# Optimization experiments

Hardware: AMD Instinct MI355X
Metric: run time of the kernel (lower is better)

The kernel has to match this reference:

```python
import jax, jax.numpy as jnp
import numpy as np

NCHARS = 50000
NWORDS = 500000
NIC = 64      # ninput_char
NIW = 64      # ninput_word
NH = 128      # nhidden
NA = 5        # naction (nmapping_fn)
B = 65536     # batch size


def setup_inputs() -> dict:
    key = jax.random.key(0)
    ks = jax.random.split(key, 12)
    s = 0.05
    return {
        "x": jax.random.randint(ks[0], (B, 2), 0, NCHARS),
        "y": jax.random.randint(ks[1], (B,), 0, NWORDS),
        "cemb_table": jax.random.normal(ks[2], (NCHARS, NIC), jnp.float32) * s,
        "wemb_table": jax.random.normal(ks[3], (NWORDS, NIW), jnp.float32) * s,
        # Policy MLP: Linear(2*NIC -> NH), ReLU, Linear(NH -> NA), Softmax
        "Wp1": jax.random.normal(ks[4], (2 * NIC, NH), jnp.float32) * s,
        "bp1": jnp.zeros((NH,), jnp.float32),
        "Wp2": jax.random.normal(ks[5], (NH, NA), jnp.float32) * s,
        "bp2": jnp.zeros((NA,), jnp.float32),
        # NA expert MLPs, stacked: Linear(2*NIC -> NH), ReLU, Linear(NH -> NIW)
        "We1": jax.random.normal(ks[6], (NA, 2 * NIC, NH), jnp.float32) * s,
        "be1": jnp.zeros((NA, NH), jnp.float32),
        "We2": jax.random.normal(ks[7], (NA, NH, NIW), jnp.float32) * s,
        "be2": jnp.zeros((NA, NIW), jnp.float32),
    }


def reference(x, y, cemb_table, wemb_table, Wp1, bp1, Wp2, bp2, We1, be1, We2, be2):
    bsize = x.shape[0]
    # char_embs(x).view(bsize, -1): [B, 2*NIC]
    cembs = cemb_table[x].reshape(bsize, -1)

    # Policy (dropout off in eval): probs = softmax(relu(cembs@Wp1+bp1)@Wp2+bp2)
    # Categorical sampling over probs == categorical over the pre-softmax logits.
    logits = jnp.maximum(cembs @ Wp1 + bp1, 0.0) @ Wp2 + bp2
    action = jax.random.categorical(jax.random.key(42), logits)   # [B]
    action_mask = jax.nn.one_hot(action, NA, dtype=cembs.dtype)   # [B, NA]

    # Dense evaluation of all NA experts (matches the Python loop + stack)
    h = jnp.maximum(jnp.einsum('bd,adh->bah', cembs, We1) + be1, 0.0)  # [B, NA, NH]
    mapped = jnp.einsum('bah,aho->bao', h, We2) + be2                  # [B, NA, NIW]

    # sum(unsqueeze(mask,-1) * mapped, dim=1)
    out = jnp.einsum('ba,bao->bo', action_mask, mapped)               # [B, NIW]

    wemb = wemb_table[y]                                              # [B, NIW]
    return (out, wemb)
```

## Files before the change

### kernel.cpp

```cpp
#include <hip/hip_runtime.h>
#include <stdint.h>

#define B_N   65536
#define NIC   64
#define NIW   64
#define NH    128
#define NA    5
#define D2    128

#define PARTITIONABLE 1

#define P2_NCHUNK 51
#define P2_R      1286

typedef __attribute__((ext_vector_type(8))) short short8;
typedef __attribute__((ext_vector_type(4))) float f32x4;

__device__ __forceinline__ ushort f2bf(float f) {
  uint32_t u = __float_as_uint(f);
  uint32_t r = (u + 0x7FFFu + ((u >> 16) & 1u)) >> 16;
  return (ushort)r;
}

__device__ __forceinline__ void split2(float f, ushort& h, ushort& l) {
  h = f2bf(f);
  l = f2bf(f - __uint_as_float(((uint32_t)h) << 16));
}

__device__ __forceinline__ void threefry2x32_k042(uint32_t x0, uint32_t x1,
                                                  uint32_t& o0, uint32_t& o1) {
  const uint32_t ks0 = 0u;
  const uint32_t ks1 = 42u;
  const uint32_t ks2 = 0x1BD11BDAu ^ 0u ^ 42u;
  x0 += ks0; x1 += ks1;
#define TF_RND(r) { x0 += x1; x1 = (x1 << (r)) | (x1 >> (32 - (r))); x1 ^= x0; }
  TF_RND(13) TF_RND(15) TF_RND(26) TF_RND(6)
  x0 += ks1; x1 += ks2 + 1u;
  TF_RND(17) TF_RND(29) TF_RND(16) TF_RND(24)
  x0 += ks2; x1 += ks0 + 2u;
  TF_RND(13) TF_RND(15) TF_RND(26) TF_RND(6)
  x0 += ks0; x1 += ks1 + 3u;
  TF_RND(17) TF_RND(29) TF_RND(16) TF_RND(24)
  x0 += ks1; x1 += ks2 + 4u;
  TF_RND(13) TF_RND(15) TF_RND(26) TF_RND(6)
  x0 += ks2; x1 += ks0 + 5u;
#undef TF_RND
  o0 = x0; o1 = x1;
}

__device__ __forceinline__ float gumbel_at(uint32_t idx) {
  uint32_t bits;
#if PARTITIONABLE
  uint32_t a, b;
  threefry2x32_k042(0u, idx, a, b);
  bits = a ^ b;
#else
  const uint32_t HALF = (uint32_t)(B_N * NA) / 2u;
  uint32_t a, b;
  if (idx < HALF) { threefry2x32_k042(idx, idx + HALF, a, b); bits = a; }
  else            { threefry2x32_k042(idx - HALF, idx, a, b); bits = b; }
#endif
  const float f = __uint_as_float((bits >> 9) | 0x3f800000u) - 1.0f;
  const double u = (f == 0.0f) ? (double)0x1p-126 : (double)f;
  const float nl = (float)(-log(u));
  const float g  = (float)(-log((double)nl));
  return g;
}

__global__ __launch_bounds__(512, 4) void policy_kernel(
    const int* __restrict__ x, const int* __restrict__ y,
    const float* __restrict__ cemb, const float* __restrict__ wemb,
    const float* __restrict__ Wp1, const float* __restrict__ bp1,
    const float* __restrict__ Wp2, const float* __restrict__ bp2,
    float* __restrict__ out_wemb, int* __restrict__ action) {
  __shared__ __align__(16) ushort sW1h[16384];
  __shared__ __align__(16) ushort sW1l[16384];
  __shared__ __align__(16) float sW2t[NA][NH];
  __shared__ __align__(16) float sb1[NH];
  __shared__ __align__(16) float sbp2[8];

  const int tid = threadIdx.x;
  const int base = blockIdx.x * 128;

  {
    const int n = tid & 127, q = tid >> 7;
    const int fb = (n >> 4) * 4 + q;
    const int cc = n & 15;
#pragma unroll
    for (int grp = 0; grp < 4; grp++) {
      short8 ph, pl;
#pragma unroll
      for (int j = 0; j < 8; j++) {
        const int k = 32 * q + 8 * grp + j;
        ushort hh, ll;
        split2(Wp1[k * NH + n], hh, ll);
        ph[j] = (short)hh;
        pl[j] = (short)ll;
      }
      *(short8*)&sW1h[fb * 512 + (cc + 16 * grp) * 8] = ph;
      *(short8*)&sW1l[fb * 512 + (cc + 16 * grp) * 8] = pl;
    }
    if (tid < NH) sb1[tid] = bp1[tid];
    if (tid < NA * 32) {
      const int a = tid >> 5, k0 = (tid & 31) * 4;
#pragma unroll
      for (int j = 0; j < 4; j++) sW2t[a][k0 + j] = Wp2[(k0 + j) * NA + a];
    }
    if (tid < NA) sbp2[tid] = bp2[tid];
  }

  const int wave = tid >> 6, lane = tid & 63;
  const int c16 = lane & 15, h2 = lane >> 4;

  const int grow = base + wave * 16 + c16;
  const int xi0 = x[grow * 2], xi1 = x[grow * 2 + 1];
  short8 Ah[4], Al[4];
#pragma unroll
  for (int kt = 0; kt < 4; kt++) {
    const int xi = (kt < 2) ? xi0 : xi1;
    const float* src = cemb + (size_t)xi * NIC + (kt & 1) * 32 + h2 * 8;
    const float4 aa = *(const float4*)src;
    const float4 bb = *(const float4*)(src + 4);
    ushort hh, ll;
    short8 ph, pl;
    split2(aa.x, hh, ll); ph[0] = (short)hh; pl[0] = (short)ll;
    split2(aa.y, hh, ll); ph[1] = (short)hh; pl[1] = (short)ll;
    split2(aa.z, hh, ll); ph[2] = (short)hh; pl[2] = (short)ll;
    split2(aa.w, hh, ll); ph[3] = (short)hh; pl[3] = (short)ll;
    split2(bb.x, hh, ll); ph[4] = (short)hh; pl[4] = (short)ll;
    split2(bb.y, hh, ll); ph[5] = (short)hh; pl[5] = (short)ll;
    split2(bb.z, hh, ll); ph[6] = (short)hh; pl[6] = (short)ll;
    split2(bb.w, hh, ll); ph[7] = (short)hh; pl[7] = (short)ll;
    Ah[kt] = ph;
    Al[kt] = pl;
  }
  __syncthreads();

  float part[4][5];
#pragma unroll
  for (int r = 0; r < 4; r++)
#pragma unroll
    for (int a = 0; a < NA; a++) part[r][a] = 0.0f;

#pragma unroll
  for (int half = 0; half < 2; half++) {
    f32x4 acc[4];
#pragma unroll
    for (int c2 = 0; c2 < 4; c2++) {
      const float bv = sb1[(half * 4 + c2) * 16 + c16];
      acc[c2] = (f32x4){bv, bv, bv, bv};
    }
#pragma unroll
    for (int kt = 0; kt < 4; kt++) {
#pragma unroll
      for (int c2 = 0; c2 < 4; c2++) {
        const int fb = (half * 4 + c2) * 4 + kt;
        const short8 Bh = *(const short8*)&sW1h[fb * 512 + lane * 8];
        const short8 Bl = *(const short8*)&sW1l[fb * 512 + lane * 8];
        acc[c2] = __builtin_amdgcn_mfma_f32_16x16x32_bf16(Ah[kt], Bh, acc[c2], 0, 0, 0);
        acc[c2] = __builtin_amdgcn_mfma_f32_16x16x32_bf16(Al[kt], Bh, acc[c2], 0, 0, 0);
        acc[c2] = __builtin_amdgcn_mfma_f32_16x16x32_bf16(Ah[kt], Bl, acc[c2], 0, 0, 0);
      }
    }
#pragma unroll
    for (int c2 = 0; c2 < 4; c2++) {
      const int ct = half * 4 + c2;
      float w[NA];
#pragma unroll
      for (int a = 0; a < NA; a++) w[a] = sW2t[a][ct * 16 + c16];
#pragma unroll
      for (int r = 0; r < 4; r++) {
        const float hv = fmaxf(acc[c2][r], 0.0f);
#pragma unroll
        for (int a = 0; a < NA; a++) part[r][a] = fmaf(hv, w[a], part[r][a]);
      }
    }
  }

#pragma unroll
  for (int st = 1; st <= 8; st <<= 1) {
#pragma unroll
    for (int r = 0; r < 4; r++)
#pragma unroll
      for (int a = 0; a < NA; a++)
        part[r][a] += __shfl_xor(part[r][a], st);
  }

  float score0, score1;
  {
    const int r0_ = c16 / 5, a0_ = c16 - 5 * (c16 / 5);
    float lg = 0.0f;
#pragma unroll
    for (int r = 0; r < 4; r++)
#pragma unroll
      for (int a = 0; a < NA; a++)
        if (r0_ == r && a0_ == a) lg = part[r][a];
    const float logit = lg + sbp2[a0_];
    const int growr = base + wave * 16 + h2 * 4 + r0_;
    score0 = gumbel_at((uint32_t)(growr * NA + a0_)) + logit;
  }
  {
    const int a1_ = (c16 & 3) + 1;
    float lg = 0.0f;
#pragma unroll
    for (int a = 1; a < NA; a++)
      if (a1_ == a) lg = part[3][a];
    const float logit = lg + sbp2[a1_];
    const int growr = base + wave * 16 + h2 * 4 + 3;
    score1 = gumbel_at((uint32_t)(growr * NA + a1_)) + logit;
  }

  int best = 0;
  float bs = 0.0f;
#pragma unroll
  for (int a = 0; a < NA; a++) {
    const int idx = c16 * 5 + a;
    const int src = h2 * 16 + ((idx < 16) ? idx : (idx - 16));
    const float v0 = __shfl(score0, src);
    const float v1 = __shfl(score1, src);
    const float s = (idx < 16) ? v0 : v1;
    if (a == 0) bs = s;
    else if (s > bs) { bs = s; best = a; }
  }
  if (c16 < 4) action[base + wave * 16 + h2 * 4 + c16] = best;

#pragma unroll 1
  for (int i = tid; i < 128 * 16; i += 512) {
    const int row = i >> 4, seg = i & 15;
    ((float4*)out_wemb)[(size_t)(base + row) * 16 + seg] =
        ((const float4*)wemb)[(size_t)y[base + row] * 16 + seg];
  }
}

__global__ __launch_bounds__(512, 1) void expert_staged(
    const int* __restrict__ x, const float* __restrict__ cemb,
    const float* __restrict__ We1, const float* __restrict__ be1,
    const float* __restrict__ We2, const float* __restrict__ be2,
    const int* __restrict__ action, float* __restrict__ out) {
  __shared__ __align__(16) ushort sW1[16384];
  __shared__ __align__(16) ushort sW2[8192];
  __shared__ __align__(16) ushort sHt[8][2048];
  __shared__ __align__(16) float sbe1[NH];
  __shared__ __align__(16) float sbe2[NIW];
  __shared__ int sList[P2_R];
  __shared__ int sCount;

  const int tid = threadIdx.x;
  const int a = blockIdx.x % NA;
  const int chunk = blockIdx.x / NA;
  const int rowBeg = chunk * P2_R;
  const int rowEnd = (rowBeg + P2_R < B_N) ? rowBeg + P2_R : B_N;

  const int wave = tid >> 6, lane = tid & 63;

  if (tid == 0) sCount = 0;
  __syncthreads();

  for (int r0 = rowBeg; r0 < rowEnd; r0 += 512) {
    const int r = r0 + tid;
    const bool m = (r < rowEnd) && (action[r] == a);
    const unsigned long long mask = __ballot(m);
    const int wcnt = __popcll(mask);
    int wbase = 0;
    if (lane == 0 && wcnt) wbase = atomicAdd(&sCount, wcnt);
    wbase = __shfl(wbase, 0);
    if (m)
      sList[wbase + __popcll(mask & ((1ull << lane) - 1ull))] = r;
  }

  {
    const float* W1g = We1 + (size_t)a * D2 * NH;
    const int n = tid & 127, q = tid >> 7;
    const int fb = (n >> 4) * 4 + q;
    const int cc = n & 15;
#pragma unroll
    for (int grp = 0; grp < 4; grp++) {
      short8 pk;
#pragma unroll
      for (int j = 0; j < 8; j++)
        pk[j] = (short)f2bf(W1g[(32 * q + 8 * grp + j) * NH + n]);
      *(short8*)&sW1[fb * 512 + (cc + 16 * grp) * 8] = pk;
    }
    if (tid < NH) sbe1[tid] = be1[a * NH + tid];
    if (tid < NIW) sbe2[tid] = be2[a * NIW + tid];
  }
  {
    const float* W2g = We2 + (size_t)a * NH * NIW;
    const int o = tid & 63, hq = tid >> 6;
    const int fb = (o >> 4) * 4 + (hq >> 1);
    const int cc = o & 15;
#pragma unroll
    for (int g2 = 0; g2 < 2; g2++) {
      const int grp = (hq & 1) * 2 + g2;
      short8 pk;
#pragma unroll
      for (int j = 0; j < 8; j++)
        pk[j] = (short)f2bf(W2g[(16 * hq + 8 * g2 + j) * NIW + o]);
      *(short8*)&sW2[fb * 512 + (cc + 16 * grp) * 8] = pk;
    }
  }
  __syncthreads();

  const int cnt = sCount;
  if (cnt == 0) return;

  const int c16 = lane & 15, h2 = lane >> 4;
  const int rowb = h2 * 4;
  ushort* myHt = sHt[wave];

#pragma unroll 1
  for (int t16 = wave * 16; t16 < cnt; t16 += 128) {
    const int slot = t16 + c16;
    const int g = sList[(slot < cnt) ? slot : 0];
    const int2 xi2 = ((const int2*)x)[g];
    short8 Ae[4];
#pragma unroll
    for (int kt = 0; kt < 4; kt++) {
      const float* src = cemb + (size_t)((kt < 2) ? xi2.x : xi2.y) * NIC +
                         (kt & 1) * 32 + h2 * 8;
      const float4 aa = *(const float4*)src;
      const float4 bb = *(const float4*)(src + 4);
      short8 pk;
      pk[0] = (short)f2bf(aa.x); pk[1] = (short)f2bf(aa.y);
      pk[2] = (short)f2bf(aa.z); pk[3] = (short)f2bf(aa.w);
      pk[4] = (short)f2bf(bb.x); pk[5] = (short)f2bf(bb.y);
      pk[6] = (short)f2bf(bb.z); pk[7] = (short)f2bf(bb.w);
      Ae[kt] = pk;
    }

#pragma unroll
    for (int ct = 0; ct < 8; ct++) {
      const int n = ct * 16 + c16;
      const float bv = sbe1[n];
      f32x4 acc = {bv, bv, bv, bv};
#pragma unroll
      for (int kt = 0; kt < 4; kt++) {
        const short8 Bf = *(const short8*)&sW1[(ct * 4 + kt) * 512 + lane * 8];
        acc = __builtin_amdgcn_mfma_f32_16x16x32_bf16(Ae[kt], Bf, acc, 0, 0, 0);
      }
      const int kt2 = n >> 5, grp2 = (n & 31) >> 3, j2 = n & 7;
#pragma unroll
      for (int r = 0; r < 4; r++)
        myHt[kt2 * 512 + ((rowb + r) + 16 * grp2) * 8 + j2] =
            f2bf(fmaxf(acc[r], 0.0f));
    }

    short8 A2[4];
#pragma unroll
    for (int kt = 0; kt < 4; kt++)
      A2[kt] = *(const short8*)&myHt[kt * 512 + lane * 8];
    int gr4[4];
#pragma unroll
    for (int r = 0; r < 4; r++) {
      const int li2 = t16 + rowb + r;
      gr4[r] = (li2 < cnt) ? sList[li2] : -1;
    }
#pragma unroll
    for (int ot = 0; ot < 4; ot++) {
      const int o = ot * 16 + c16;
      const float bv = sbe2[o];
      f32x4 o4 = {bv, bv, bv, bv};
#pragma unroll
      for (int kt = 0; kt < 4; kt++) {
        const short8 Bf = *(const short8*)&sW2[(ot * 4 + kt) * 512 + lane * 8];
        o4 = __builtin_amdgcn_mfma_f32_16x16x32_bf16(A2[kt], Bf, o4, 0, 0, 0);
      }
#pragma unroll
      for (int r = 0; r < 4; r++)
        if (gr4[r] >= 0) out[(size_t)gr4[r] * NIW + o] = o4[r];
    }
  }
}

extern "C" void kernel_launch(void* const* d_in, const int* in_sizes, int n_in,
                              void* d_out, int out_size, void* d_ws, size_t ws_size,
                              hipStream_t stream) {
  const int*   x    = (const int*)d_in[0];
  const int*   y    = (const int*)d_in[1];
  const float* cemb = (const float*)d_in[2];
  const float* wemb = (const float*)d_in[3];
  const float* Wp1  = (const float*)d_in[4];
  const float* bp1  = (const float*)d_in[5];
  const float* Wp2  = (const float*)d_in[6];
  const float* bp2  = (const float*)d_in[7];
  const float* We1  = (const float*)d_in[8];
  const float* be1  = (const float*)d_in[9];
  const float* We2  = (const float*)d_in[10];
  const float* be2  = (const float*)d_in[11];

  float* out      = (float*)d_out;
  float* out_wemb = out + (size_t)B_N * NIW;
  int*   action   = (int*)d_ws;

  policy_kernel<<<B_N / 128, 512, 0, stream>>>(
      x, y, cemb, wemb, Wp1, bp1, Wp2, bp2, out_wemb, action);
  expert_staged<<<NA * P2_NCHUNK, 512, 0, stream>>>(
      x, cemb, We1, be1, We2, be2, action, out);
}
```

Baseline: 41.73 us.

## Pre-pack expert weights in policy kernel and prefetch next embedding tile

Five extra blocks added to the policy launch convert each expert's We1/We2 to bf16 in MFMA fragment layout and write them to workspace. The expert kernel then copies the packed weights with vector loads into LDS before building its row list, instead of doing strided fp32 loads and conversion in each of its 255 blocks. The expert loop also software-pipelines the cemb gather, loading the next tile's raw rows into registers while the current tile computes. The policy kernel reads x as int2. This costs more registers and workspace memory, plus a global round-trip of the packed weights between the two kernels.

```diff
diff --git a/kernel.cpp b/kernel.cpp
--- a/kernel.cpp
+++ b/kernel.cpp
@@ -10,8 +10,11 @@
 
 #define PARTITIONABLE 1
 
+#define NBLK      512
 #define P2_NCHUNK 51
 #define P2_R      1286
+
+#define WS_ACTION_BYTES  262144
 
 typedef __attribute__((ext_vector_type(8))) short short8;
 typedef __attribute__((ext_vector_type(4))) float f32x4;
@@ -72,7 +75,9 @@
     const float* __restrict__ cemb, const float* __restrict__ wemb,
     const float* __restrict__ Wp1, const float* __restrict__ bp1,
     const float* __restrict__ Wp2, const float* __restrict__ bp2,
-    float* __restrict__ out_wemb, int* __restrict__ action) {
+    const float* __restrict__ We1, const float* __restrict__ We2,
+    float* __restrict__ out_wemb, int* __restrict__ action,
+    ushort* __restrict__ wPrep) {
   __shared__ __align__(16) ushort sW1h[16384];
   __shared__ __align__(16) ushort sW1l[16384];
   __shared__ __align__(16) float sW2t[NA][NH];
@@ -80,6 +85,42 @@
   __shared__ __align__(16) float sbp2[8];
 
   const int tid = threadIdx.x;
+
+  if (blockIdx.x >= NBLK) {
+    const int a = blockIdx.x - NBLK;
+    ushort* wp = wPrep + (size_t)a * 24576;
+    {
+      const float* W1g = We1 + (size_t)a * D2 * NH;
+      const int n = tid & 127, q = tid >> 7;
+      const int fb = (n >> 4) * 4 + q;
+      const int cc = n & 15;
+#pragma unroll
+      for (int grp = 0; grp < 4; grp++) {
+        short8 pk;
+#pragma unroll
+        for (int j = 0; j < 8; j++)
+          pk[j] = (short)f2bf(W1g[(32 * q + 8 * grp + j) * NH + n]);
+        *(short8*)&wp[fb * 512 + (cc + 16 * grp) * 8] = pk;
+      }
+    }
+    {
+      const float* W2g = We2 + (size_t)a * NH * NIW;
+      const int o = tid & 63, hq = tid >> 6;
+      const int fb = (o >> 4) * 4 + (hq >> 1);
+      const int cc = o & 15;
+#pragma unroll
+      for (int g2 = 0; g2 < 2; g2++) {
+        const int grp = (hq & 1) * 2 + g2;
+        short8 pk;
+#pragma unroll
+        for (int j = 0; j < 8; j++)
+          pk[j] = (short)f2bf(W2g[(16 * hq + 8 * g2 + j) * NIW + o]);
+        *(short8*)&wp[16384 + fb * 512 + (cc + 16 * grp) * 8] = pk;
+      }
+    }
+    return;
+  }
+
   const int base = blockIdx.x * 128;
 
   {
@@ -113,7 +154,8 @@
   const int c16 = lane & 15, h2 = lane >> 4;
 
   const int grow = base + wave * 16 + c16;
-  const int xi0 = x[grow * 2], xi1 = x[grow * 2 + 1];
+  const int2 xi2p = ((const int2*)x)[grow];
+  const int xi0 = xi2p.x, xi1 = xi2p.y;
   short8 Ah[4], Al[4];
 #pragma unroll
   for (int kt = 0; kt < 4; kt++) {
@@ -234,9 +276,9 @@
 
 __global__ __launch_bounds__(512, 1) void expert_staged(
     const int* __restrict__ x, const float* __restrict__ cemb,
-    const float* __restrict__ We1, const float* __restrict__ be1,
-    const float* __restrict__ We2, const float* __restrict__ be2,
-    const int* __restrict__ action, float* __restrict__ out) {
+    const float* __restrict__ be1, const float* __restrict__ be2,
+    const int* __restrict__ action, const ushort* __restrict__ wPrep,
+    float* __restrict__ out) {
   __shared__ __align__(16) ushort sW1[16384];
   __shared__ __align__(16) ushort sW2[8192];
   __shared__ __align__(16) ushort sHt[8][2048];
@@ -255,6 +297,19 @@
 
   if (tid == 0) sCount = 0;
   __syncthreads();
+
+  {
+    const short8* s1 = (const short8*)(wPrep + (size_t)a * 24576);
+    const short8* s2 = s1 + 2048;
+    short8* d1 = (short8*)sW1;
+    short8* d2 = (short8*)sW2;
+#pragma unroll
+    for (int i = 0; i < 4; i++) d1[tid + i * 512] = s1[tid + i * 512];
+#pragma unroll
+    for (int i = 0; i < 2; i++) d2[tid + i * 512] = s2[tid + i * 512];
+    if (tid < NH) sbe1[tid] = be1[a * NH + tid];
+    if (tid < NIW) sbe2[tid] = be2[a * NIW + tid];
+  }
 
   for (int r0 = rowBeg; r0 < rowEnd; r0 += 512) {
     const int r = r0 + tid;
@@ -267,38 +322,6 @@
     if (m)
       sList[wbase + __popcll(mask & ((1ull << lane) - 1ull))] = r;
   }
-
-  {
-    const float* W1g = We1 + (size_t)a * D2 * NH;
-    const int n = tid & 127, q = tid >> 7;
-    const int fb = (n >> 4) * 4 + q;
-    const int cc = n & 15;
-#pragma unroll
-    for (int grp = 0; grp < 4; grp++) {
-      short8 pk;
-#pragma unroll
-      for (int j = 0; j < 8; j++)
-        pk[j] = (short)f2bf(W1g[(32 * q + 8 * grp + j) * NH + n]);
-      *(short8*)&sW1[fb * 512 + (cc + 16 * grp) * 8] = pk;
-    }
-    if (tid < NH) sbe1[tid] = be1[a * NH + tid];
-    if (tid < NIW) sbe2[tid] = be2[a * NIW + tid];
-  }
-  {
-    const float* W2g = We2 + (size_t)a * NH * NIW;
-    const int o = tid & 63, hq = tid >> 6;
-    const int fb = (o >> 4) * 4 + (hq >> 1);
-    const int cc = o & 15;
-#pragma unroll
-    for (int g2 = 0; g2 < 2; g2++) {
-      const int grp = (hq & 1) * 2 + g2;
-      short8 pk;
-#pragma unroll
-      for (int j = 0; j < 8; j++)
-        pk[j] = (short)f2bf(W2g[(16 * hq + 8 * g2 + j) * NIW + o]);
-      *(short8*)&sW2[fb * 512 + (cc + 16 * grp) * 8] = pk;
-    }
-  }
   __syncthreads();
 
   const int cnt = sCount;
@@ -308,18 +331,31 @@
   const int rowb = h2 * 4;
   ushort* myHt = sHt[wave];
 
-#pragma unroll 1
-  for (int t16 = wave * 16; t16 < cnt; t16 += 128) {
+  int t16 = wave * 16;
+  if (t16 >= cnt) return;
+
+  float4 raw[8];
+  {
     const int slot = t16 + c16;
     const int g = sList[(slot < cnt) ? slot : 0];
     const int2 xi2 = ((const int2*)x)[g];
-    short8 Ae[4];
 #pragma unroll
     for (int kt = 0; kt < 4; kt++) {
       const float* src = cemb + (size_t)((kt < 2) ? xi2.x : xi2.y) * NIC +
                          (kt & 1) * 32 + h2 * 8;
-      const float4 aa = *(const float4*)src;
-      const float4 bb = *(const float4*)(src + 4);
+      raw[2 * kt]     = *(const float4*)src;
+      raw[2 * kt + 1] = *(const float4*)(src + 4);
+    }
+  }
+
+#pragma unroll 1
+  while (t16 < cnt) {
+    const int tn = t16 + 128;
+
+    short8 Ae[4];
+#pragma unroll
+    for (int kt = 0; kt < 4; kt++) {
+      const float4 aa = raw[2 * kt], bb = raw[2 * kt + 1];
       short8 pk;
       pk[0] = (short)f2bf(aa.x); pk[1] = (short)f2bf(aa.y);
       pk[2] = (short)f2bf(aa.z); pk[3] = (short)f2bf(aa.w);
@@ -328,6 +364,19 @@
       Ae[kt] = pk;
     }
 
+    if (tn < cnt) {
+      const int slot = tn + c16;
+      const int g = sList[(slot < cnt) ? slot : 0];
+      const int2 xi2 = ((const int2*)x)[g];
+#pragma unroll
+      for (int kt = 0; kt < 4; kt++) {
+        const float* src = cemb + (size_t)((kt < 2) ? xi2.x : xi2.y) * NIC +
+                           (kt & 1) * 32 + h2 * 8;
+        raw[2 * kt]     = *(const float4*)src;
+        raw[2 * kt + 1] = *(const float4*)(src + 4);
+      }
+    }
+
 #pragma unroll
     for (int ct = 0; ct < 8; ct++) {
       const int n = ct * 16 + c16;
@@ -369,6 +418,8 @@
       for (int r = 0; r < 4; r++)
         if (gr4[r] >= 0) out[(size_t)gr4[r] * NIW + o] = o4[r];
     }
+
+    t16 = tn;
   }
 }
 
@@ -390,10 +441,11 @@
 
   float* out      = (float*)d_out;
   float* out_wemb = out + (size_t)B_N * NIW;
-  int*   action   = (int*)d_ws;
-
-  policy_kernel<<<B_N / 128, 512, 0, stream>>>(
-      x, y, cemb, wemb, Wp1, bp1, Wp2, bp2, out_wemb, action);
+  int*    action  = (int*)d_ws;
+  ushort* wPrep   = (ushort*)((char*)d_ws + WS_ACTION_BYTES);
+
+  policy_kernel<<<NBLK + NA, 512, 0, stream>>>(
+      x, y, cemb, wemb, Wp1, bp1, Wp2, bp2, We1, We2, out_wemb, action, wPrep);
   expert_staged<<<NA * P2_NCHUNK, 512, 0, stream>>>(
-      x, cemb, We1, be1, We2, be2, action, out);
-}
+      x, cemb, be1, be2, action, wPrep, out);
+}
```

Result: no change. 42.21 us (+1.2%).
